# Kernel tuning notes

Measured on AMD Instinct MI355X. Metric: run time of the kernel, lower is better.

Reference implementation:

```python
import jax, jax.numpy as jnp
import numpy as np

DIM = 2048
N_HEADS = 16
HEAD_DIM = DIM // N_HEADS  # 128
HIDDEN = 8192
EPS = 1e-6
NEG = -1e9


def rmsnorm(x, w):
    xf = x.astype(jnp.float32)
    y = xf * jax.lax.rsqrt(jnp.mean(xf * xf, axis=-1, keepdims=True) + EPS)
    return y.astype(x.dtype) * w


def apply_rope(x, cos, sin):
    # x: [B,S,H,Hd]; cos/sin: [S,Hd//2] -> broadcast [1,S,1,Hd//2]
    xf = x.astype(jnp.float32)
    xr = xf[..., 0::2]
    xi = xf[..., 1::2]
    c = cos[None, :, None, :]
    s = sin[None, :, None, :]
    or_ = xr * c - xi * s
    oi_ = xr * s + xi * c
    out = jnp.stack([or_, oi_], axis=-1).reshape(x.shape)
    return out.astype(x.dtype)


def setup_inputs() -> dict:
    key = jax.random.key(0)
    ks = jax.random.split(key, 10)
    B, S = 1, 2048
    x = jax.random.normal(ks[0], (B, S, DIM), dtype=jnp.float32)
    # RoPE frequencies (Llama-style, theta=10000)
    inv_freq = 1.0 / (10000.0 ** (jnp.arange(0, HEAD_DIM, 2, dtype=jnp.float32) / HEAD_DIM))
    angles = jnp.arange(S, dtype=jnp.float32)[:, None] * inv_freq[None, :]  # [S, Hd//2]
    freqs_cos = jnp.cos(angles)
    freqs_sin = jnp.sin(angles)
    # causal additive mask [1,1,S,S]
    mask = jnp.where(jnp.tril(jnp.ones((S, S), dtype=bool)), 0.0, NEG).astype(jnp.float32)[None, None]
    sc = 0.02
    wq = jax.random.normal(ks[1], (DIM, DIM), dtype=jnp.float32) * sc
    wk = jax.random.normal(ks[2], (DIM, DIM), dtype=jnp.float32) * sc
    wv = jax.random.normal(ks[3], (DIM, DIM), dtype=jnp.float32) * sc
    wo = jax.random.normal(ks[4], (DIM, DIM), dtype=jnp.float32) * sc
    w1 = jax.random.normal(ks[5], (DIM, HIDDEN), dtype=jnp.float32) * sc
    w2 = jax.random.normal(ks[6], (HIDDEN, DIM), dtype=jnp.float32) * sc
    w3 = jax.random.normal(ks[7], (DIM, HIDDEN), dtype=jnp.float32) * sc
    attn_norm_w = jnp.ones((DIM,), dtype=jnp.float32)
    ffn_norm_w = jnp.ones((DIM,), dtype=jnp.float32)
    return {"x": x, "freqs_cos": freqs_cos, "freqs_sin": freqs_sin, "mask": mask,
            "wq": wq, "wk": wk, "wv": wv, "wo": wo, "w1": w1, "w2": w2, "w3": w3,
            "attn_norm_w": attn_norm_w, "ffn_norm_w": ffn_norm_w}


def reference(x, freqs_cos, freqs_sin, mask, wq, wk, wv, wo, w1, w2, w3, attn_norm_w, ffn_norm_w):
    B, S, D = x.shape
    # --- attention (pre-norm) ---
    hn = rmsnorm(x, attn_norm_w)
    q = (hn @ wq).reshape(B, S, N_HEADS, HEAD_DIM)
    k = (hn @ wk).reshape(B, S, N_HEADS, HEAD_DIM)
    v = (hn @ wv).reshape(B, S, N_HEADS, HEAD_DIM)
    q = apply_rope(q, freqs_cos, freqs_sin)
    k = apply_rope(k, freqs_cos, freqs_sin)
    scores = jnp.einsum('bqhd,bkhd->bhqk', q, k) / (HEAD_DIM ** 0.5) + mask
    attn = jax.nn.softmax(scores.astype(jnp.float32), axis=-1).astype(q.dtype)
    ctx = jnp.einsum('bhqk,bkhd->bqhd', attn, v).reshape(B, S, D)
    h = x + ctx @ wo
    # --- SwiGLU FFN (pre-norm) ---
    fn = rmsnorm(h, ffn_norm_w)
    ff = (jax.nn.silu(fn @ w1) * (fn @ w3)) @ w2
    return h + ff
```

## Files before the change

kernel.cpp:

```cpp
#include <hip/hip_runtime.h>
#include <hip/hip_bf16.h>

#define DIM 2048
#define HEAD_DIM 128
#define N_HEADS 16
#define SEQ 2048
#define HID 8192
#define SQKV 6144

typedef short bf16x8 __attribute__((ext_vector_type(8)));
typedef float f32x4 __attribute__((ext_vector_type(4)));
using bf16 = __hip_bfloat16;

#define MFMA16(a, b, c) __builtin_amdgcn_mfma_f32_16x16x32_bf16(a, b, c, 0, 0, 0)

__device__ __forceinline__ unsigned short f2bu(float f) {
    union { bf16 b; unsigned short u; } cv;
    cv.b = __float2bfloat16(f);
    return cv.u;
}

__device__ __forceinline__ void gl16(const void* g, void* l) {
    __builtin_amdgcn_global_load_lds(
        (const __attribute__((address_space(1))) unsigned int*)g,
        (__attribute__((address_space(3))) unsigned int*)l, 16, 0, 0);
}

__global__ __launch_bounds__(256) void rmsnorm_bf16_k(
    const float* __restrict__ x, const float* __restrict__ w, bf16* __restrict__ y)
{
    const int row = blockIdx.x;
    const int tid = threadIdx.x;
    const float* xr = x + (size_t)row * DIM;
    float4 v0 = ((const float4*)xr)[tid];
    float4 v1 = ((const float4*)xr)[tid + 256];
    float ss = v0.x*v0.x + v0.y*v0.y + v0.z*v0.z + v0.w*v0.w
             + v1.x*v1.x + v1.y*v1.y + v1.z*v1.z + v1.w*v1.w;
    for (int o = 32; o > 0; o >>= 1) ss += __shfl_down(ss, o);
    __shared__ float red[4];
    if ((tid & 63) == 0) red[tid >> 6] = ss;
    __syncthreads();
    float tot = red[0] + red[1] + red[2] + red[3];
    float r = rsqrtf(tot * (1.0f / DIM) + 1e-6f);
    float4 w0 = ((const float4*)w)[tid];
    float4 w1 = ((const float4*)w)[tid + 256];
    ushort4 o0, o1;
    o0.x = f2bu(v0.x * r * w0.x); o0.y = f2bu(v0.y * r * w0.y);
    o0.z = f2bu(v0.z * r * w0.z); o0.w = f2bu(v0.w * r * w0.w);
    o1.x = f2bu(v1.x * r * w1.x); o1.y = f2bu(v1.y * r * w1.y);
    o1.z = f2bu(v1.z * r * w1.z); o1.w = f2bu(v1.w * r * w1.w);
    ushort4* yr = (ushort4*)(y + (size_t)row * DIM);
    yr[tid] = o0;
    yr[tid + 256] = o1;
}

__global__ __launch_bounds__(256) void rmsnorm4_k(
    const float* __restrict__ part, const float* __restrict__ x,
    const float* __restrict__ w, float* __restrict__ hout, bf16* __restrict__ y)
{
    const int row = blockIdx.x;
    const int tid = threadIdx.x;
    const size_t base = (size_t)row * DIM;
    const size_t SP = (size_t)SEQ * DIM;
    float4 r0, r1;
    float ss = 0.0f;
    {
        float4 a  = ((const float4*)(x + base))[tid];
        float4 p0 = ((const float4*)(part + base))[tid];
        float4 p1 = ((const float4*)(part + SP + base))[tid];
        float4 p2 = ((const float4*)(part + 2 * SP + base))[tid];
        float4 p3 = ((const float4*)(part + 3 * SP + base))[tid];
        r0.x = a.x + ((p0.x + p1.x) + (p2.x + p3.x));
        r0.y = a.y + ((p0.y + p1.y) + (p2.y + p3.y));
        r0.z = a.z + ((p0.z + p1.z) + (p2.z + p3.z));
        r0.w = a.w + ((p0.w + p1.w) + (p2.w + p3.w));
        ((float4*)(hout + base))[tid] = r0;
        ss += r0.x*r0.x + r0.y*r0.y + r0.z*r0.z + r0.w*r0.w;
    }
    {
        const int t2 = tid + 256;
        float4 a  = ((const float4*)(x + base))[t2];
        float4 p0 = ((const float4*)(part + base))[t2];
        float4 p1 = ((const float4*)(part + SP + base))[t2];
        float4 p2 = ((const float4*)(part + 2 * SP + base))[t2];
        float4 p3 = ((const float4*)(part + 3 * SP + base))[t2];
        r1.x = a.x + ((p0.x + p1.x) + (p2.x + p3.x));
        r1.y = a.y + ((p0.y + p1.y) + (p2.y + p3.y));
        r1.z = a.z + ((p0.z + p1.z) + (p2.z + p3.z));
        r1.w = a.w + ((p0.w + p1.w) + (p2.w + p3.w));
        ((float4*)(hout + base))[t2] = r1;
        ss += r1.x*r1.x + r1.y*r1.y + r1.z*r1.z + r1.w*r1.w;
    }
    for (int o = 32; o > 0; o >>= 1) ss += __shfl_down(ss, o);
    __shared__ float red[4];
    if ((tid & 63) == 0) red[tid >> 6] = ss;
    __syncthreads();
    float tot = red[0] + red[1] + red[2] + red[3];
    float r = rsqrtf(tot * (1.0f / DIM) + 1e-6f);
    float4 w0 = ((const float4*)w)[tid];
    float4 w1 = ((const float4*)w)[tid + 256];
    ushort4 o0, o1;
    o0.x = f2bu(r0.x * r * w0.x); o0.y = f2bu(r0.y * r * w0.y);
    o0.z = f2bu(r0.z * r * w0.z); o0.w = f2bu(r0.w * r * w0.w);
    o1.x = f2bu(r1.x * r * w1.x); o1.y = f2bu(r1.y * r * w1.y);
    o1.z = f2bu(r1.z * r * w1.z); o1.w = f2bu(r1.w * r * w1.w);
    ushort4* yr = (ushort4*)(y + base);
    yr[tid] = o0;
    yr[tid + 256] = o1;
}

__global__ __launch_bounds__(256) void reduce4_k(
    const float* __restrict__ part, const float* __restrict__ h, float* __restrict__ out)
{
    const size_t i = (size_t)blockIdx.x * 256 + threadIdx.x;
    const size_t SP4 = (size_t)SEQ * DIM / 4;
    float4 a  = ((const float4*)h)[i];
    float4 p0 = ((const float4*)part)[i];
    float4 p1 = ((const float4*)part)[i + SP4];
    float4 p2 = ((const float4*)part)[i + 2 * SP4];
    float4 p3 = ((const float4*)part)[i + 3 * SP4];
    float4 r;
    r.x = a.x + ((p0.x + p1.x) + (p2.x + p3.x));
    r.y = a.y + ((p0.y + p1.y) + (p2.y + p3.y));
    r.z = a.z + ((p0.z + p1.z) + (p2.z + p3.z));
    r.w = a.w + ((p0.w + p1.w) + (p2.w + p3.w));
    ((float4*)out)[i] = r;
}

__global__ __launch_bounds__(256) void convT_f32_bf16_k(
    const float* __restrict__ in, bf16* __restrict__ out, int R, int C)
{
    __shared__ float t[32][33];
    const int tx = threadIdx.x, ty = threadIdx.y;
    const int x0 = blockIdx.x * 32, y0 = blockIdx.y * 32;
#pragma unroll
    for (int i = 0; i < 4; ++i)
        t[ty + i * 8][tx] = in[(size_t)(y0 + ty + i * 8) * C + x0 + tx];
    __syncthreads();
#pragma unroll
    for (int i = 0; i < 4; ++i)
        out[(size_t)(x0 + ty + i * 8) * R + y0 + tx] = __float2bfloat16(t[tx][ty + i * 8]);
}

__global__ __launch_bounds__(256) void convT3_f32_bf16_k(
    const float* __restrict__ wq, const float* __restrict__ wk,
    const float* __restrict__ wv, bf16* __restrict__ out)
{
    const int z = blockIdx.z;
    const float* in = z == 0 ? wq : (z == 1 ? wk : wv);
    bf16* o = out + (size_t)z * DIM * DIM;
    __shared__ float t[32][33];
    const int tx = threadIdx.x, ty = threadIdx.y;
    const int x0 = blockIdx.x * 32, y0 = blockIdx.y * 32;
#pragma unroll
    for (int i = 0; i < 4; ++i)
        t[ty + i * 8][tx] = in[(size_t)(y0 + ty + i * 8) * DIM + x0 + tx];
    __syncthreads();
#pragma unroll
    for (int i = 0; i < 4; ++i)
        o[(size_t)(x0 + ty + i * 8) * DIM + y0 + tx] = __float2bfloat16(t[tx][ty + i * 8]);
}

__global__ __launch_bounds__(256) void transpose_bf16_k(
    const bf16* __restrict__ in, int istride, bf16* __restrict__ out)
{
    __shared__ unsigned short t[32][33];
    const int tx = threadIdx.x, ty = threadIdx.y;
    const int x = blockIdx.x * 32 + tx;
    const int y0 = blockIdx.y * 32;
    const unsigned short* inu = (const unsigned short*)in;
    unsigned short* outu = (unsigned short*)out;
#pragma unroll
    for (int i = 0; i < 4; ++i)
        t[ty + i * 8][tx] = inu[(size_t)(y0 + ty + i * 8) * istride + x];
    __syncthreads();
    const int x2 = blockIdx.y * 32 + tx;
    const int y2 = blockIdx.x * 32;
#pragma unroll
    for (int i = 0; i < 4; ++i)
        outu[(size_t)(y2 + ty + i * 8) * SEQ + x2] = t[tx][ty + i * 8];
}

__global__ __launch_bounds__(256) void rope_qk_k(
    bf16* __restrict__ q, bf16* __restrict__ k,
    const float* __restrict__ cosb, const float* __restrict__ sinb)
{
    const int gid = blockIdx.x * 256 + threadIdx.x;
    const int s = gid >> 10;
    const int p = gid & 1023;
    const int h = p >> 6, j = p & 63;
    const size_t off = (size_t)s * SQKV + h * HEAD_DIM + 2 * j;
    const float c = cosb[s * 64 + j], sn = sinb[s * 64 + j];
    float xr = __bfloat162float(q[off]), xi = __bfloat162float(q[off + 1]);
    q[off]     = __float2bfloat16(xr * c - xi * sn);
    q[off + 1] = __float2bfloat16(xr * sn + xi * c);
    xr = __bfloat162float(k[off]); xi = __bfloat162float(k[off + 1]);
    k[off]     = __float2bfloat16(xr * c - xi * sn);
    k[off + 1] = __float2bfloat16(xr * sn + xi * c);
}

template <int EP>
__global__ __launch_bounds__(512, 2) void gemm256_k(
    const bf16* __restrict__ A, const bf16* __restrict__ Bt,
    bf16* __restrict__ Cb, const bf16* other, float* __restrict__ Pf,
    int M, int N, int K, int gx, int ntile, int Ks)
{
    extern __shared__ char smem[];
    const int t512 = threadIdx.x;
    const int w = t512 >> 6, lane = t512 & 63;
    const int lr = lane & 15, lg = lane >> 4;
    const int wm = w >> 2, wn = w & 3;
    const int bofs = (wn & 1) * 64;

    const int nwg = gridDim.x;
    const int q8 = nwg >> 3, r8 = nwg & 7;
    const int xcd = blockIdx.x & 7, seq = blockIdx.x >> 3;
    const int wgid = (xcd < r8 ? xcd * (q8 + 1) : r8 * (q8 + 1) + (xcd - r8) * q8) + seq;
    const int split = wgid / ntile;
    const int tile = wgid % ntile;
    const int grp = tile / (4 * gx), rem = tile % (4 * gx);
    const int m0 = (grp * 4 + (rem & 3)) * 256, n0 = (rem >> 2) * 256;
    const int kb0 = split * Ks;

    const int nt = Ks >> 6;

    auto stage_half = [&](int buf, int kt, int isB, int hs) {
        const int k0 = kb0 + (kt << 6);
        char* base = smem + (isB ? 65536 : 0) + (buf * 2 + hs) * 16384;
#pragma unroll
        for (int c = 0; c < 2; ++c) {
            const int s = (c * 512 + t512) * 16;
            const int p = s ^ (((s >> 7) & 7) << 4);
            const int row = p >> 7;
            const int colE = (p & 127) >> 1;
            if (isB)
                gl16(Bt + (size_t)(n0 + hs * 128 + row) * K + k0 + colE, base + s);
            else
                gl16(A  + (size_t)(m0 + hs * 128 + row) * K + k0 + colE, base + s);
        }
    };

    f32x4 acc[8][4] = {};
    bf16x8 bfr[4][2];

    stage_half(0, 0, 0, 0); stage_half(0, 0, 0, 1);
    stage_half(0, 0, 1, 0); stage_half(0, 0, 1, 1);
    stage_half(1, 1, 0, 0); stage_half(1, 1, 0, 1);
    stage_half(1, 1, 1, 0); stage_half(1, 1, 1, 1);

    for (int t = 0; t < nt; ++t) {
        const int cur = t & 1;
        if (t + 1 < nt) { asm volatile("s_waitcnt vmcnt(8)" ::: "memory"); }
        else            { asm volatile("s_waitcnt vmcnt(0)" ::: "memory"); }
        __builtin_amdgcn_sched_barrier(0);
        __builtin_amdgcn_s_barrier();

        const char* Am = smem + (cur * 2 + wm) * 16384;
        const char* Bm = smem + 65536 + (cur * 2 + (wn >> 1)) * 16384;
        const bool pf = (t + 2 < nt);

#define LDA_(mf, ks, dst) { int off = (((mf) * 16 + lr) * 128) + ((((ks) * 64) + lg * 16) ^ ((lr & 7) << 4)); \
        dst = *(const bf16x8*)(Am + off); }
#define LDB_(nf, ks, dst) { int off = ((bofs + (nf) * 16 + lr) * 128) + ((((ks) * 64) + lg * 16) ^ ((lr & 7) << 4)); \
        dst = *(const bf16x8*)(Bm + off); }
#define MFMA_PH(mf0) { \
        asm volatile("s_waitcnt lgkmcnt(0)" ::: "memory"); \
        __builtin_amdgcn_sched_barrier(0); \
        __builtin_amdgcn_s_setprio(1); \
        _Pragma("unroll") \
        for (int nf = 0; nf < 4; ++nf) { \
            acc[(mf0)][nf]     = MFMA16(a0, bfr[nf][0], acc[(mf0)][nf]); \
            acc[(mf0)][nf]     = MFMA16(a1, bfr[nf][1], acc[(mf0)][nf]); \
            acc[(mf0) + 1][nf] = MFMA16(a2, bfr[nf][0], acc[(mf0) + 1][nf]); \
            acc[(mf0) + 1][nf] = MFMA16(a3, bfr[nf][1], acc[(mf0) + 1][nf]); \
        } \
        __builtin_amdgcn_s_setprio(0); }

        bf16x8 a0, a1, a2, a3;
        LDA_(0, 0, a0) LDA_(0, 1, a1) LDA_(1, 0, a2) LDA_(1, 1, a3)
#pragma unroll
        for (int nf = 0; nf < 4; ++nf) { LDB_(nf, 0, bfr[nf][0]) LDB_(nf, 1, bfr[nf][1]) }
        MFMA_PH(0)
        __builtin_amdgcn_s_barrier();
        if (pf) stage_half(cur, t + 2, 1, 0);

        LDA_(2, 0, a0) LDA_(2, 1, a1) LDA_(3, 0, a2) LDA_(3, 1, a3)
        MFMA_PH(2)
        __builtin_amdgcn_s_barrier();
        if (pf) stage_half(cur, t + 2, 1, 1);

        LDA_(4, 0, a0) LDA_(4, 1, a1) LDA_(5, 0, a2) LDA_(5, 1, a3)
        MFMA_PH(4)

        LDA_(6, 0, a0) LDA_(6, 1, a1) LDA_(7, 0, a2) LDA_(7, 1, a3)
        MFMA_PH(6)
        __builtin_amdgcn_s_barrier();
        if (pf) { stage_half(cur, t + 2, 0, 0); stage_half(cur, t + 2, 0, 1); }
#undef LDA_
#undef LDB_
#undef MFMA_PH
    }

    float* pf_base = Pf + (size_t)split * M * N;
#pragma unroll
    for (int mf = 0; mf < 8; ++mf)
#pragma unroll
        for (int nf = 0; nf < 4; ++nf) {
            const int row = m0 + wm * 128 + mf * 16 + lg * 4;
            const int col = n0 + wn * 64 + nf * 16 + lr;
#pragma unroll
            for (int r = 0; r < 4; ++r) {
                const size_t idx = (size_t)(row + r) * N + col;
                const float v = acc[mf][nf][r];
                if (EP == 0) {
                    Cb[idx] = __float2bfloat16(v);
                } else if (EP == 2) {
                    const float gg = __bfloat162float(other[idx]);
                    const float sg = gg / (1.0f + __expf(-gg));
                    Cb[idx] = __float2bfloat16(sg * v);
                } else {
                    pf_base[idx] = v;
                }
            }
        }
}

__global__ __launch_bounds__(256) void attn_fwd_k(
    const bf16* __restrict__ qkv, const bf16* __restrict__ vT, bf16* __restrict__ ctx)
{
    const int tid = threadIdx.x;
    const int w = tid >> 6, lane = tid & 63;
    const int lr = lane & 15, lg = lane >> 4;
    const int h = blockIdx.y;
    const int qidx = (blockIdx.y < 8) ? blockIdx.x : (31 - blockIdx.x);
    const int q0b = qidx * 64;
    const int nt = qidx + 1;

    __shared__ __align__(16) unsigned short Kt[2][64 * 128];
    __shared__ __align__(16) unsigned short Vt[2][128 * 64];
    __shared__ __align__(16) unsigned short Pp[4][16 * 64];

    const char* kbase = (const char*)(qkv + DIM + h * HEAD_DIM);
    const char* vbase = (const char*)(vT + (size_t)h * HEAD_DIM * SEQ);

    const int krow_c = tid >> 4;
    const int kcolB  = (tid & 15) * 16;
    const int vrow_c = tid >> 3;
    const int vcolB  = (tid & 7) * 16;

    auto stage = [&](int buf, int kb) {
#pragma unroll
        for (int c = 0; c < 4; ++c) {
            const int r = c * 16 + krow_c;
            gl16(kbase + (size_t)(kb + r) * (SQKV * 2) + (kcolB ^ ((r & 7) << 4)),
                 &Kt[buf][c * 2048 + tid * 8]);
        }
#pragma unroll
        for (int c = 0; c < 4; ++c) {
            const int r = c * 32 + vrow_c;
            gl16(vbase + (size_t)r * (SEQ * 2) + kb * 2 + (vcolB ^ ((r & 7) << 4)),
                 &Vt[buf][c * 2048 + tid * 8]);
        }
    };

    bf16x8 qf[4];
    const bf16* qrow = qkv + (size_t)(q0b + w * 16 + lr) * SQKV + h * HEAD_DIM;
#pragma unroll
    for (int dt = 0; dt < 4; ++dt)
        qf[dt] = *(const bf16x8*)(qrow + dt * 32 + lg * 8);

    f32x4 o[8] = {};
    float m[4], l[4];
#pragma unroll
    for (int j = 0; j < 4; ++j) { m[j] = -3e38f; l[j] = 0.0f; }
    const float scale = 0.08838834764831845f;

    stage(0, 0);
    __syncthreads();

    int cur = 0;
    for (int t = 0; t < nt; ++t) {
        const int kb = t * 64;
        if (t + 1 < nt) stage(cur ^ 1, kb + 64);

        f32x4 s[4] = {};
        __builtin_amdgcn_s_setprio(1);
#pragma unroll
        for (int ss = 0; ss < 4; ++ss) {
            const int r = ss * 16 + lr;
            const int sw = (r & 7) << 3;
#pragma unroll
            for (int dt = 0; dt < 4; ++dt) {
                bf16x8 kf = *(const bf16x8*)&Kt[cur][r * 128 + ((dt * 32 + lg * 8) ^ sw)];
                s[ss] = MFMA16(qf[dt], kf, s[ss]);
            }
        }
        __builtin_amdgcn_s_setprio(0);

        float al[4];
#pragma unroll
        for (int j = 0; j < 4; ++j) {
            const int qi = q0b + w * 16 + lg * 4 + j;
            const int prow = lg * 4 + j;
            const int psw = (prow & 7) << 3;
            float a[4];
#pragma unroll
            for (int ss = 0; ss < 4; ++ss)
                a[ss] = s[ss][j] * scale + ((kb + ss * 16 + lr) > qi ? -1e9f : 0.0f);
            float mx = fmaxf(fmaxf(a[0], a[1]), fmaxf(a[2], a[3]));
            mx = fmaxf(mx, __shfl_xor(mx, 1));
            mx = fmaxf(mx, __shfl_xor(mx, 2));
            mx = fmaxf(mx, __shfl_xor(mx, 4));
            mx = fmaxf(mx, __shfl_xor(mx, 8));
            const float mn = fmaxf(m[j], mx);
            const float asc = __expf(m[j] - mn);
            float e0 = __expf(a[0] - mn), e1 = __expf(a[1] - mn);
            float e2 = __expf(a[2] - mn), e3 = __expf(a[3] - mn);
            float rs = (e0 + e1) + (e2 + e3);
            rs += __shfl_xor(rs, 1); rs += __shfl_xor(rs, 2);
            rs += __shfl_xor(rs, 4); rs += __shfl_xor(rs, 8);
            l[j] = l[j] * asc + rs;
            m[j] = mn;
            al[j] = asc;
            Pp[w][prow * 64 + ((lr)      ^ psw)] = f2bu(e0);
            Pp[w][prow * 64 + ((16 + lr) ^ psw)] = f2bu(e1);
            Pp[w][prow * 64 + ((32 + lr) ^ psw)] = f2bu(e2);
            Pp[w][prow * 64 + ((48 + lr) ^ psw)] = f2bu(e3);
        }
#pragma unroll
        for (int d2 = 0; d2 < 8; ++d2)
#pragma unroll
            for (int j = 0; j < 4; ++j) o[d2][j] *= al[j];

        asm volatile("s_waitcnt lgkmcnt(0)" ::: "memory");
        __builtin_amdgcn_sched_barrier(0);
        const int asw = (lr & 7) << 3;
        bf16x8 pa0 = *(const bf16x8*)&Pp[w][lr * 64 + ((lg * 8)      ^ asw)];
        bf16x8 pa1 = *(const bf16x8*)&Pp[w][lr * 64 + ((32 + lg * 8) ^ asw)];

        __builtin_amdgcn_s_setprio(1);
#pragma unroll
        for (int d2 = 0; d2 < 8; ++d2) {
            const int rv = d2 * 16 + lr;
            const int vsw = (rv & 7) << 3;
            bf16x8 vf0 = *(const bf16x8*)&Vt[cur][rv * 64 + ((lg * 8)      ^ vsw)];
            bf16x8 vf1 = *(const bf16x8*)&Vt[cur][rv * 64 + ((32 + lg * 8) ^ vsw)];
            o[d2] = MFMA16(pa0, vf0, o[d2]);
            o[d2] = MFMA16(pa1, vf1, o[d2]);
        }
        __builtin_amdgcn_s_setprio(0);

        __syncthreads();
        cur ^= 1;
    }

#pragma unroll
    for (int j = 0; j < 4; ++j) {
        const float inv = 1.0f / l[j];
        bf16* dst = ctx + (size_t)(q0b + w * 16 + lg * 4 + j) * DIM + h * HEAD_DIM + lr;
#pragma unroll
        for (int d2 = 0; d2 < 8; ++d2)
            dst[d2 * 16] = __float2bfloat16(o[d2][j] * inv);
    }
}

extern "C" void kernel_launch(void* const* d_in, const int* in_sizes, int n_in,
                              void* d_out, int out_size, void* d_ws, size_t ws_size,
                              hipStream_t stream)
{
    const float* x   = (const float*)d_in[0];
    const float* fc  = (const float*)d_in[1];
    const float* fs  = (const float*)d_in[2];
    const float* wq  = (const float*)d_in[4];
    const float* wk  = (const float*)d_in[5];
    const float* wv  = (const float*)d_in[6];
    const float* wo  = (const float*)d_in[7];
    const float* w1  = (const float*)d_in[8];
    const float* w2  = (const float*)d_in[9];
    const float* w3  = (const float*)d_in[10];
    const float* anw = (const float*)d_in[11];
    const float* fnw = (const float*)d_in[12];
    float* out = (float*)d_out;

    char* p = (char*)d_ws;
    auto alloc = [&](size_t n) { char* r = p; p += (n + 255) & ~(size_t)255; return r; };
    bf16* wT  = (bf16*)alloc((size_t)HID * DIM * 2);
    bf16* hn  = (bf16*)alloc((size_t)SEQ * DIM * 2);
    bf16* qkv = (bf16*)alloc((size_t)SEQ * SQKV * 2);
    bf16* vt  = (bf16*)alloc((size_t)SEQ * DIM * 2);
    bf16* ctx = (bf16*)alloc((size_t)SEQ * DIM * 2);
    bf16* fn  = (bf16*)alloc((size_t)SEQ * DIM * 2);
    float* h  = (float*)alloc((size_t)SEQ * DIM * 4);
    bf16* g   = (bf16*)alloc((size_t)SEQ * HID * 2);
    float* sk = (float*)alloc((size_t)4 * SEQ * DIM * 4);

    const dim3 tb32(32, 8);
    const int LDS256 = 131072;
    (void)hipFuncSetAttribute((const void*)gemm256_k<0>,
        hipFuncAttributeMaxDynamicSharedMemorySize, LDS256);
    (void)hipFuncSetAttribute((const void*)gemm256_k<2>,
        hipFuncAttributeMaxDynamicSharedMemorySize, LDS256);
    (void)hipFuncSetAttribute((const void*)gemm256_k<3>,
        hipFuncAttributeMaxDynamicSharedMemorySize, LDS256);

    rmsnorm_bf16_k<<<SEQ, 256, 0, stream>>>(x, anw, hn);

    convT3_f32_bf16_k<<<dim3(DIM / 32, DIM / 32, 3), tb32, 0, stream>>>(wq, wk, wv, wT);
    gemm256_k<0><<<(SEQ / 256) * (SQKV / 256), 512, LDS256, stream>>>(
        hn, wT, qkv, nullptr, nullptr, SEQ, SQKV, DIM, SQKV / 256, (SEQ / 256) * (SQKV / 256), DIM);

    rope_qk_k<<<(SEQ * 1024) / 256, 256, 0, stream>>>(qkv, qkv + DIM, fc, fs);
    transpose_bf16_k<<<dim3(DIM / 32, SEQ / 32), tb32, 0, stream>>>(qkv + 2 * DIM, SQKV, vt);

    attn_fwd_k<<<dim3(SEQ / 64, N_HEADS), 256, 0, stream>>>(qkv, vt, ctx);

    convT_f32_bf16_k<<<dim3(DIM / 32, DIM / 32), tb32, 0, stream>>>(wo, wT, DIM, DIM);
    gemm256_k<3><<<(SEQ / 256) * (DIM / 256) * 4, 512, LDS256, stream>>>(
        ctx, wT, nullptr, nullptr, sk, SEQ, DIM, DIM, DIM / 256, (SEQ / 256) * (DIM / 256), 512);
    rmsnorm4_k<<<SEQ, 256, 0, stream>>>(sk, x, fnw, h, fn);

    convT_f32_bf16_k<<<dim3(HID / 32, DIM / 32), tb32, 0, stream>>>(w1, wT, DIM, HID);
    gemm256_k<0><<<(SEQ / 256) * (HID / 256), 512, LDS256, stream>>>(
        fn, wT, g, nullptr, nullptr, SEQ, HID, DIM, HID / 256, (SEQ / 256) * (HID / 256), DIM);
    convT_f32_bf16_k<<<dim3(HID / 32, DIM / 32), tb32, 0, stream>>>(w3, wT, DIM, HID);
    gemm256_k<2><<<(SEQ / 256) * (HID / 256), 512, LDS256, stream>>>(
        fn, wT, g, g, nullptr, SEQ, HID, DIM, HID / 256, (SEQ / 256) * (HID / 256), DIM);

    convT_f32_bf16_k<<<dim3(DIM / 32, HID / 32), tb32, 0, stream>>>(w2, wT, HID, DIM);
    gemm256_k<3><<<(SEQ / 256) * (DIM / 256) * 4, 512, LDS256, stream>>>(
        g, wT, nullptr, nullptr, sk, SEQ, DIM, HID, DIM / 256, (SEQ / 256) * (DIM / 256), 2048);
    reduce4_k<<<(SEQ * DIM / 4) / 256, 256, 0, stream>>>(sk, h, out);
}
```

Before: 521.6 us.

## Double-buffer A fragments in GEMM main loop and precompute staging pointers

Restructures the 256x256 GEMM inner loop so A-fragment LDS reads for the next MFMA phase are issued before the current phase, using two register sets and partial lgkmcnt(4) waits instead of full drains. All B staging for the next k-tile is issued after the first phase, with A staging after the last. Global source pointers for async LDS staging are precomputed once, outside the loop. The aim is to hide LDS read latency behind MFMAs and cut address arithmetic, at the cost of extra VGPRs under 512-thread, 2-block launch bounds.

```diff
diff --git a/kernel.cpp b/kernel.cpp
--- a/kernel.cpp
+++ b/kernel.cpp
@@ -214,92 +214,111 @@
 
     const int nwg = gridDim.x;
     const int q8 = nwg >> 3, r8 = nwg & 7;
-    const int xcd = blockIdx.x & 7, seq = blockIdx.x >> 3;
-    const int wgid = (xcd < r8 ? xcd * (q8 + 1) : r8 * (q8 + 1) + (xcd - r8) * q8) + seq;
+    const int xcd = blockIdx.x & 7, seqq = blockIdx.x >> 3;
+    const int wgid = (xcd < r8 ? xcd * (q8 + 1) : r8 * (q8 + 1) + (xcd - r8) * q8) + seqq;
     const int split = wgid / ntile;
     const int tile = wgid % ntile;
     const int grp = tile / (4 * gx), rem = tile % (4 * gx);
     const int m0 = (grp * 4 + (rem & 3)) * 256, n0 = (rem >> 2) * 256;
     const int kb0 = split * Ks;
-
     const int nt = Ks >> 6;
 
-    auto stage_half = [&](int buf, int kt, int isB, int hs) {
-        const int k0 = kb0 + (kt << 6);
-        char* base = smem + (isB ? 65536 : 0) + (buf * 2 + hs) * 16384;
-#pragma unroll
-        for (int c = 0; c < 2; ++c) {
-            const int s = (c * 512 + t512) * 16;
-            const int p = s ^ (((s >> 7) & 7) << 4);
-            const int row = p >> 7;
-            const int colE = (p & 127) >> 1;
-            if (isB)
-                gl16(Bt + (size_t)(n0 + hs * 128 + row) * K + k0 + colE, base + s);
-            else
-                gl16(A  + (size_t)(m0 + hs * 128 + row) * K + k0 + colE, base + s);
+    const bf16* aS[2][2]; const bf16* bS[2][2];
+    int sOff[2];
+#pragma unroll
+    for (int c = 0; c < 2; ++c) {
+        const int s = (c * 512 + t512) * 16;
+        const int pp = s ^ (((s >> 7) & 7) << 4);
+        const int row = pp >> 7, colE = (pp & 127) >> 1;
+        sOff[c] = s;
+#pragma unroll
+        for (int hs = 0; hs < 2; ++hs) {
+            aS[hs][c] = A  + (size_t)(m0 + hs * 128 + row) * K + kb0 + colE;
+            bS[hs][c] = Bt + (size_t)(n0 + hs * 128 + row) * K + kb0 + colE;
+        }
+    }
+    auto stageA = [&](int buf, int kt) {
+#pragma unroll
+        for (int hs = 0; hs < 2; ++hs) {
+            char* base = smem + (buf * 2 + hs) * 16384;
+            gl16(aS[hs][0] + (kt << 6), base + sOff[0]);
+            gl16(aS[hs][1] + (kt << 6), base + sOff[1]);
+        }
+    };
+    auto stageB = [&](int buf, int kt) {
+#pragma unroll
+        for (int hs = 0; hs < 2; ++hs) {
+            char* base = smem + 65536 + (buf * 2 + hs) * 16384;
+            gl16(bS[hs][0] + (kt << 6), base + sOff[0]);
+            gl16(bS[hs][1] + (kt << 6), base + sOff[1]);
         }
     };
 
     f32x4 acc[8][4] = {};
     bf16x8 bfr[4][2];
 
-    stage_half(0, 0, 0, 0); stage_half(0, 0, 0, 1);
-    stage_half(0, 0, 1, 0); stage_half(0, 0, 1, 1);
-    stage_half(1, 1, 0, 0); stage_half(1, 1, 0, 1);
-    stage_half(1, 1, 1, 0); stage_half(1, 1, 1, 1);
+    stageB(0, 0); stageA(0, 0);
+    stageB(1, 1); stageA(1, 1);
+
+#define SB __builtin_amdgcn_sched_barrier(0)
+#define WAITL4 SB; asm volatile("s_waitcnt lgkmcnt(4)" ::: "memory"); SB
+#define WAITL0 SB; asm volatile("s_waitcnt lgkmcnt(0)" ::: "memory"); SB
+#define LDA_(mf, ks, dst) { int off = (((mf) * 16 + lr) * 128) + ((((ks) * 64) + lg * 16) ^ ((lr & 7) << 4)); \
+        dst = *(const bf16x8*)(Am + off); }
+#define LDB_(nf, ks, dst) { int off = ((bofs + (nf) * 16 + lr) * 128) + ((((ks) * 64) + lg * 16) ^ ((lr & 7) << 4)); \
+        dst = *(const bf16x8*)(Bm + off); }
+#define MFMA_PH(mf0, r0, r1, r2, r3) { \
+        __builtin_amdgcn_s_setprio(1); \
+        _Pragma("unroll") \
+        for (int nf = 0; nf < 4; ++nf) { \
+            acc[(mf0)][nf]     = MFMA16(r0, bfr[nf][0], acc[(mf0)][nf]); \
+            acc[(mf0)][nf]     = MFMA16(r1, bfr[nf][1], acc[(mf0)][nf]); \
+            acc[(mf0) + 1][nf] = MFMA16(r2, bfr[nf][0], acc[(mf0) + 1][nf]); \
+            acc[(mf0) + 1][nf] = MFMA16(r3, bfr[nf][1], acc[(mf0) + 1][nf]); \
+        } \
+        __builtin_amdgcn_s_setprio(0); }
 
     for (int t = 0; t < nt; ++t) {
         const int cur = t & 1;
         if (t + 1 < nt) { asm volatile("s_waitcnt vmcnt(8)" ::: "memory"); }
         else            { asm volatile("s_waitcnt vmcnt(0)" ::: "memory"); }
-        __builtin_amdgcn_sched_barrier(0);
+        SB;
         __builtin_amdgcn_s_barrier();
 
         const char* Am = smem + (cur * 2 + wm) * 16384;
         const char* Bm = smem + 65536 + (cur * 2 + (wn >> 1)) * 16384;
         const bool pf = (t + 2 < nt);
 
-#define LDA_(mf, ks, dst) { int off = (((mf) * 16 + lr) * 128) + ((((ks) * 64) + lg * 16) ^ ((lr & 7) << 4)); \
-        dst = *(const bf16x8*)(Am + off); }
-#define LDB_(nf, ks, dst) { int off = ((bofs + (nf) * 16 + lr) * 128) + ((((ks) * 64) + lg * 16) ^ ((lr & 7) << 4)); \
-        dst = *(const bf16x8*)(Bm + off); }
-#define MFMA_PH(mf0) { \
-        asm volatile("s_waitcnt lgkmcnt(0)" ::: "memory"); \
-        __builtin_amdgcn_sched_barrier(0); \
-        __builtin_amdgcn_s_setprio(1); \
-        _Pragma("unroll") \
-        for (int nf = 0; nf < 4; ++nf) { \
-            acc[(mf0)][nf]     = MFMA16(a0, bfr[nf][0], acc[(mf0)][nf]); \
-            acc[(mf0)][nf]     = MFMA16(a1, bfr[nf][1], acc[(mf0)][nf]); \
-            acc[(mf0) + 1][nf] = MFMA16(a2, bfr[nf][0], acc[(mf0) + 1][nf]); \
-            acc[(mf0) + 1][nf] = MFMA16(a3, bfr[nf][1], acc[(mf0) + 1][nf]); \
-        } \
-        __builtin_amdgcn_s_setprio(0); }
-
-        bf16x8 a0, a1, a2, a3;
-        LDA_(0, 0, a0) LDA_(0, 1, a1) LDA_(1, 0, a2) LDA_(1, 1, a3)
+        bf16x8 x0, x1, x2, x3, y0, y1, y2, y3;
 #pragma unroll
         for (int nf = 0; nf < 4; ++nf) { LDB_(nf, 0, bfr[nf][0]) LDB_(nf, 1, bfr[nf][1]) }
-        MFMA_PH(0)
+        LDA_(0, 0, x0) LDA_(0, 1, x1) LDA_(1, 0, x2) LDA_(1, 1, x3)
+        SB;
+        LDA_(2, 0, y0) LDA_(2, 1, y1) LDA_(3, 0, y2) LDA_(3, 1, y3)
+        WAITL4;
+        MFMA_PH(0, x0, x1, x2, x3)
         __builtin_amdgcn_s_barrier();
-        if (pf) stage_half(cur, t + 2, 1, 0);
-
-        LDA_(2, 0, a0) LDA_(2, 1, a1) LDA_(3, 0, a2) LDA_(3, 1, a3)
-        MFMA_PH(2)
+        if (pf) stageB(cur, t + 2);
+
+        LDA_(4, 0, x0) LDA_(4, 1, x1) LDA_(5, 0, x2) LDA_(5, 1, x3)
+        WAITL4;
+        MFMA_PH(2, y0, y1, y2, y3)
+
+        LDA_(6, 0, y0) LDA_(6, 1, y1) LDA_(7, 0, y2) LDA_(7, 1, y3)
+        WAITL4;
+        MFMA_PH(4, x0, x1, x2, x3)
+
+        WAITL0;
+        MFMA_PH(6, y0, y1, y2, y3)
         __builtin_amdgcn_s_barrier();
-        if (pf) stage_half(cur, t + 2, 1, 1);
-
-        LDA_(4, 0, a0) LDA_(4, 1, a1) LDA_(5, 0, a2) LDA_(5, 1, a3)
-        MFMA_PH(4)
-
-        LDA_(6, 0, a0) LDA_(6, 1, a1) LDA_(7, 0, a2) LDA_(7, 1, a3)
-        MFMA_PH(6)
-        __builtin_amdgcn_s_barrier();
-        if (pf) { stage_half(cur, t + 2, 0, 0); stage_half(cur, t + 2, 0, 1); }
+        if (pf) stageA(cur, t + 2);
+    }
 #undef LDA_
 #undef LDB_
 #undef MFMA_PH
-    }
+#undef WAITL4
+#undef WAITL0
+#undef SB
 
     float* pf_base = Pf + (size_t)split * M * N;
 #pragma unroll
```

New measurement: 514.6 us. About the same (-1.3%).
